# Performance work log

Measured on AMD Instinct MI355X. Metric: run time of the kernel, lower is better.

Reference implementation:

```python
import jax, jax.numpy as jnp
import numpy as np
from jax import lax

B, C, H, W = 32, 64, 128, 128   # c must equal max_in_channels (see view in forward)
OUT, K = 64, 3
HIDDEN = 128


def setup_inputs() -> dict:
    key = jax.random.key(0)
    k1, k2, k3, k4, k5 = jax.random.split(key, 5)
    x = jax.random.normal(k1, (B, C, H, W), dtype=jnp.float32)
    # torch Linear default init scale ~ 1/sqrt(fan_in); use small scale for stability
    W1 = jax.random.normal(k2, (C, HIDDEN), dtype=jnp.float32) * (1.0 / np.sqrt(C))
    b1 = jax.random.normal(k3, (HIDDEN,), dtype=jnp.float32) * 0.01
    W2 = jax.random.normal(k4, (HIDDEN, OUT * C * K * K), dtype=jnp.float32) * (1.0 / np.sqrt(HIDDEN))
    b2 = jax.random.normal(k5, (OUT * C * K * K,), dtype=jnp.float32) * 0.01
    return {"x": x, "W1": W1, "b1": b1, "W2": W2, "b2": b2}


def reference(x, W1, b1, W2, b2):
    b, c, h, w = x.shape
    # per-sample channel statistics -> weight-generator MLP
    stats = jnp.mean(x, axis=(2, 3))                       # [b, c]
    hidden = jax.nn.relu(stats @ W1 + b1)                  # [b, hidden]
    weight = (hidden @ W2 + b2).reshape(b, OUT, c, K, K)   # per-sample conv kernels
    # batched per-sample conv expressed as one grouped convolution:
    # group i convolves sample i's channels with sample i's kernels
    lhs = x.reshape(1, b * c, h, w)                        # [1, b*c, H, W]
    rhs = weight.reshape(b * OUT, c, K, K)                 # [b*OUT, c, K, K]
    pad = K // 2
    out = lax.conv_general_dilated(
        lhs, rhs,
        window_strides=(1, 1),
        padding=[(pad, pad), (pad, pad)],
        feature_group_count=b,
        dimension_numbers=("NCHW", "OIHW", "NCHW"),
    )
    return out.reshape(b, OUT, h, w)
```

## Files before the change

kernel.cpp:

```cpp
#include <hip/hip_runtime.h>

typedef unsigned short u16;
typedef unsigned int   u32;
typedef __attribute__((ext_vector_type(8))) short short8v;
typedef __attribute__((ext_vector_type(4))) float float4v;
typedef __attribute__((address_space(1))) u32 g_u32;
typedef __attribute__((address_space(3))) u32 l_u32;


__device__ __forceinline__ u16 f2bf(float f) {
  u32 u = __builtin_bit_cast(u32, f);
  return (u16)((u + 0x7fffu + ((u >> 16) & 1u)) >> 16);
}

__global__ void __launch_bounds__(256) k_transpose_stats(
    const float* __restrict__ x, float* __restrict__ statsum, u16* __restrict__ xt)
{
  __shared__ u16 tile[64 * 130];
  const int b = blockIdx.x >> 7, y = blockIdx.x & 127;
  const int tid = threadIdx.x;
  const int c = tid >> 2, part = tid & 3, xb = part * 32;
  const float* src = x + (((size_t)(b * 64 + c) * 128 + y) * 128 + xb);
  float sum = 0.f;
  #pragma unroll
  for (int i = 0; i < 32; i += 4) {
    float4 v = *(const float4*)(src + i);
    sum += (v.x + v.y) + (v.z + v.w);
    ushort2 p01; p01.x = f2bf(v.x); p01.y = f2bf(v.y);
    ushort2 p23; p23.x = f2bf(v.z); p23.y = f2bf(v.w);
    *(ushort2*)&tile[c * 130 + xb + i]     = p01;
    *(ushort2*)&tile[c * 130 + xb + i + 2] = p23;
  }
  sum += __shfl_xor(sum, 1);
  sum += __shfl_xor(sum, 2);
  if (part == 0) atomicAdd(&statsum[b * 64 + c], sum);
  __syncthreads();

  uint4* xtv = (uint4*)xt;
  const size_t rowg = ((size_t)b * 130 + (y + 1)) * 1024;
  #pragma unroll
  for (int d0 = 0; d0 < 1024; d0 += 256) {
    const int d = d0 + tid;
    const int xd = d >> 3, s = d & 7;
    const int c8 = s ^ (xd & 7);
    const u16* tp = &tile[c8 * 8 * 130 + xd];
    u16 v0 = tp[0 * 130], v1 = tp[1 * 130], v2 = tp[2 * 130], v3 = tp[3 * 130];
    u16 v4 = tp[4 * 130], v5 = tp[5 * 130], v6 = tp[6 * 130], v7 = tp[7 * 130];
    uint4 g;
    g.x = (u32)v0 | ((u32)v1 << 16);
    g.y = (u32)v2 | ((u32)v3 << 16);
    g.z = (u32)v4 | ((u32)v5 << 16);
    g.w = (u32)v6 | ((u32)v7 << 16);
    xtv[rowg + d] = g;
  }
  if (y == 0 || y == 127) {
    const size_t prow = ((size_t)b * 130 + (y == 0 ? 0 : 129)) * 1024;
    uint4 z; z.x = z.y = z.z = z.w = 0u;
    #pragma unroll
    for (int d0 = 0; d0 < 1024; d0 += 256) xtv[prow + d0 + tid] = z;
  }
}

__global__ void __launch_bounds__(128) k_hidden(
    const float* __restrict__ statsum, const float* __restrict__ W1,
    const float* __restrict__ b1, float* __restrict__ hiddenT)
{
  const int b = blockIdx.x, h = threadIdx.x;
  float s = b1[h];
  #pragma unroll 4
  for (int c = 0; c < 64; ++c)
    s = fmaf(statsum[b * 64 + c] * (1.f / 16384.f), W1[c * 128 + h], s);
  hiddenT[h * 32 + b] = fmaxf(s, 0.f);
}

__global__ void __launch_bounds__(256) k_weightgen(
    const float* __restrict__ hiddenT, const float* __restrict__ W2,
    const float* __restrict__ b2, u16* __restrict__ wt)
{
  __shared__ float red[4][64][32];
  const int tid = threadIdx.x;
  const int hg = __builtin_amdgcn_readfirstlane(tid >> 6);
  const int jl = tid & 63;
  const int j = blockIdx.x * 64 + jl;

  float acc[32];
  #pragma unroll
  for (int b = 0; b < 32; ++b) acc[b] = 0.f;

  const float* __restrict__ hbase = hiddenT + hg * 32 * 32;
  const float* __restrict__ wcol  = W2 + (size_t)hg * 32 * 36864 + j;
  #pragma unroll 2
  for (int hh = 0; hh < 32; ++hh) {
    const float w = wcol[(size_t)hh * 36864];
    const float* hr = hbase + hh * 32;
    #pragma unroll
    for (int b = 0; b < 32; ++b) acc[b] = fmaf(w, hr[b], acc[b]);
  }

  #pragma unroll
  for (int b = 0; b < 32; ++b) red[hg][jl][(b + jl) & 31] = acc[b];
  __syncthreads();

  const int jr = tid & 63, b0 = (tid >> 6) * 8;
  const int jj = blockIdx.x * 64 + jr;
  const int oc = jj / 9, kidx = jj - oc * 9;
  const int o = oc >> 6, c = oc & 63, cc2 = c >> 5, cr = c & 31;
  const float bias = b2[jj];
  #pragma unroll
  for (int i = 0; i < 8; ++i) {
    const int b = b0 + i;
    const int rot = (b + jr) & 31;
    float s = bias + red[0][jr][rot] + red[1][jr][rot]
                   + red[2][jr][rot] + red[3][jr][rot];
    const size_t widx = ((size_t)(((b * 9 + kidx) * 2 + cc2) * 64 + o)) * 32 + cr;
    wt[widx] = f2bf(s);
  }
}

__global__ void __launch_bounds__(256) k_conv(
    const u16* __restrict__ xt, const u16* __restrict__ wt, float* __restrict__ out)
{
  __shared__ u16 xs[4 * 1024 * 8];
  const int blk = blockIdx.x;
  const int b = blk >> 6, r = blk & 63;
  const int y0 = r * 2;
  const int tid = threadIdx.x;

  {
    const size_t srcg = ((size_t)b * 130 + y0) * 1024;
    #pragma unroll
    for (int k2 = 0; k2 < 16; ++k2) {
      const int g = k2 * 256 + tid;
      const void* gsrc = (const char*)xt + (srcg + (size_t)g) * 16;
      void* ldst = (char*)xs + (size_t)g * 16;
#if defined(__has_builtin) && __has_builtin(__builtin_amdgcn_global_load_lds)
      __builtin_amdgcn_global_load_lds((const g_u32*)gsrc, (l_u32*)ldst, 16, 0, 0);
#else
      *(uint4*)ldst = *(const uint4*)gsrc;
#endif
    }
  }
  __syncthreads();

  const int lane = tid & 63, wid = tid >> 6;
  const int lo = lane & 15, q = lane >> 4;
  const int yout = y0 + (wid >> 1);
  const int colbase = (wid & 1) * 64;

  const short8v z8 = {0, 0, 0, 0, 0, 0, 0, 0};
  float4v acc[4][4];
  {
    const float4v z4 = {0.f, 0.f, 0.f, 0.f};
    #pragma unroll
    for (int mt = 0; mt < 4; ++mt)
      #pragma unroll
      for (int nt = 0; nt < 4; ++nt) acc[mt][nt] = z4;
  }

  const size_t wbase = (size_t)b * 36864 + (size_t)(lo * 32 + q * 8);
  short8v a_cur[4];
  {
    const u16* p = wt + wbase;
    #pragma unroll
    for (int mt = 0; mt < 4; ++mt) a_cur[mt] = *(const short8v*)(p + mt * 512);
  }

  #pragma unroll 1
  for (int chunk = 0; chunk < 18; ++chunk) {
    const int kidx = chunk >> 1, cc = chunk & 1;
    const int ky = kidx / 3, kx = kidx - ky * 3;

    short8v a_nxt[4];
    if (chunk < 17) {
      const u16* p = wt + wbase + (size_t)(chunk + 1) * 2048;
      #pragma unroll
      for (int mt = 0; mt < 4; ++mt) a_nxt[mt] = *(const short8v*)(p + mt * 512);
    }

    const int row_l = (wid >> 1) + ky;
    const int c8 = cc * 4 + q;
    short8v bv[4];
    #pragma unroll
    for (int nt = 0; nt < 4; ++nt) {
      const int xin = colbase + nt * 16 + lo + kx - 1;
      const bool okx = ((unsigned)xin < 128u);
      const int gpos = okx ? (row_l * 1024 + xin * 8 + (c8 ^ (xin & 7))) : 0;
      short8v v = *(const short8v*)(xs + (size_t)gpos * 8);
      bv[nt] = okx ? v : z8;
    }

    #pragma unroll
    for (int mt = 0; mt < 4; ++mt)
      #pragma unroll
      for (int nt = 0; nt < 4; ++nt)
        acc[mt][nt] = __builtin_amdgcn_mfma_f32_16x16x32_bf16(
            a_cur[mt], bv[nt], acc[mt][nt], 0, 0, 0);

    if (chunk < 17) {
      #pragma unroll
      for (int mt = 0; mt < 4; ++mt) a_cur[mt] = a_nxt[mt];
    }
  }

  #pragma unroll
  for (int mt = 0; mt < 4; ++mt) {
    #pragma unroll
    for (int i = 0; i < 4; ++i) {
      const int o = mt * 16 + q * 4 + i;
      float* orow = out + ((size_t)(b * 64 + o) * 128 + yout) * 128;
      #pragma unroll
      for (int nt = 0; nt < 4; ++nt)
        orow[colbase + nt * 16 + lo] = acc[mt][nt][i];
    }
  }
}

extern "C" void kernel_launch(void* const* d_in, const int* in_sizes, int n_in,
                              void* d_out, int out_size, void* d_ws, size_t ws_size,
                              hipStream_t stream) {
  (void)in_sizes; (void)n_in; (void)out_size; (void)ws_size;
  const float* x  = (const float*)d_in[0];
  const float* W1 = (const float*)d_in[1];
  const float* b1 = (const float*)d_in[2];
  const float* W2 = (const float*)d_in[3];
  const float* b2 = (const float*)d_in[4];
  float* out = (float*)d_out;

  float* statsum = (float*)d_ws;
  float* hiddenT = (float*)((char*)d_ws + 8192);
  u16*   wt      = (u16*)((char*)d_ws + 32768);
  u16*   xt      = (u16*)((char*)d_ws + (size_t)(4 << 20));

  hipMemsetAsync(statsum, 0, 2048 * sizeof(float), stream);
  k_transpose_stats<<<32 * 128, 256, 0, stream>>>(x, statsum, xt);
  k_hidden<<<32, 128, 0, stream>>>(statsum, W1, b1, hiddenT);
  k_weightgen<<<576, 256, 0, stream>>>(hiddenT, W2, b2, wt);
  k_conv<<<32 * 64, 256, 0, stream>>>(xt, wt, out);
}
```

Measured before the change: 335.1 us.

## Overlap conv LDS tile fill with compute and triple-buffer weight fragments

In the conv kernel, the full __syncthreads after the async global-to-LDS fill becomes a partial vmcnt(8) wait plus barrier. Compute on the ky=0 chunks, which only need the first two staged rows, can then start while the last two rows are still arriving. A second vmcnt(0) barrier comes before the chunks that read the later rows. The weight-fragment loop is fully unrolled with a three-deep register rotation (A0/A1/A2) instead of a one-ahead prefetch, so global weight loads have more time to land before the MFMAs use them. The cost is higher VGPR pressure and reliance on hand-placed waitcnts. In-order vmcnt accounting may also limit the real overlap, since any compiler-inserted wait for the new weight loads also waits for the earlier LDS loads.

New measurement: 337.0 us. About the same (+0.5%).

```diff
diff --git a/kernel.cpp b/kernel.cpp
--- a/kernel.cpp
+++ b/kernel.cpp
@@ -140,7 +140,9 @@
 #endif
     }
   }
-  __syncthreads();
+  asm volatile("s_waitcnt vmcnt(8)" ::: "memory");
+  __builtin_amdgcn_s_barrier();
+  __builtin_amdgcn_sched_barrier(0);
 
   const int lane = tid & 63, wid = tid >> 6;
   const int lo = lane & 15, q = lane >> 4;
@@ -158,25 +160,16 @@
   }
 
   const size_t wbase = (size_t)b * 36864 + (size_t)(lo * 32 + q * 8);
-  short8v a_cur[4];
-  {
-    const u16* p = wt + wbase;
-    #pragma unroll
-    for (int mt = 0; mt < 4; ++mt) a_cur[mt] = *(const short8v*)(p + mt * 512);
-  }
-
-  #pragma unroll 1
-  for (int chunk = 0; chunk < 18; ++chunk) {
+
+  short8v A0[4], A1[4], A2[4];
+  auto loadA = [&](short8v* dst, int chunk) {
+    const u16* p = wt + wbase + (size_t)chunk * 2048;
+    #pragma unroll
+    for (int mt = 0; mt < 4; ++mt) dst[mt] = *(const short8v*)(p + mt * 512);
+  };
+  auto doChunk = [&](const short8v* A, int chunk) {
     const int kidx = chunk >> 1, cc = chunk & 1;
     const int ky = kidx / 3, kx = kidx - ky * 3;
-
-    short8v a_nxt[4];
-    if (chunk < 17) {
-      const u16* p = wt + wbase + (size_t)(chunk + 1) * 2048;
-      #pragma unroll
-      for (int mt = 0; mt < 4; ++mt) a_nxt[mt] = *(const short8v*)(p + mt * 512);
-    }
-
     const int row_l = (wid >> 1) + ky;
     const int c8 = cc * 4 + q;
     short8v bv[4];
@@ -188,19 +181,39 @@
       short8v v = *(const short8v*)(xs + (size_t)gpos * 8);
       bv[nt] = okx ? v : z8;
     }
-
     #pragma unroll
     for (int mt = 0; mt < 4; ++mt)
       #pragma unroll
       for (int nt = 0; nt < 4; ++nt)
         acc[mt][nt] = __builtin_amdgcn_mfma_f32_16x16x32_bf16(
-            a_cur[mt], bv[nt], acc[mt][nt], 0, 0, 0);
-
-    if (chunk < 17) {
-      #pragma unroll
-      for (int mt = 0; mt < 4; ++mt) a_cur[mt] = a_nxt[mt];
-    }
-  }
+            A[mt], bv[nt], acc[mt][nt], 0, 0, 0);
+  };
+
+  loadA(A0, 0); loadA(A1, 1); loadA(A2, 2);
+
+  doChunk(A0, 0); loadA(A0, 3);
+  doChunk(A1, 1); loadA(A1, 4);
+  doChunk(A2, 2); loadA(A2, 5);
+  doChunk(A0, 3); loadA(A0, 6);
+  doChunk(A1, 4); loadA(A1, 7);
+  doChunk(A2, 5); loadA(A2, 8);
+
+  asm volatile("s_waitcnt vmcnt(0)" ::: "memory");
+  __builtin_amdgcn_s_barrier();
+  __builtin_amdgcn_sched_barrier(0);
+
+  doChunk(A0, 6);  loadA(A0, 9);
+  doChunk(A1, 7);  loadA(A1, 10);
+  doChunk(A2, 8);  loadA(A2, 11);
+  doChunk(A0, 9);  loadA(A0, 12);
+  doChunk(A1, 10); loadA(A1, 13);
+  doChunk(A2, 11); loadA(A2, 14);
+  doChunk(A0, 12); loadA(A0, 15);
+  doChunk(A1, 13); loadA(A1, 16);
+  doChunk(A2, 14); loadA(A2, 17);
+  doChunk(A0, 15);
+  doChunk(A1, 16);
+  doChunk(A2, 17);
 
   #pragma unroll
   for (int mt = 0; mt < 4; ++mt) {
```
